# Optimization experiments

Measured on AMD Instinct MI355X. Metric: run time of the kernel, lower is better.

## Reference

```python
import jax, jax.numpy as jnp
import numpy as np

H = 64  # hidden_size
IN = 1  # input_size
OUT = 32  # fc output


def _lstm_layer(x, Wih, Whh, bih, bhh):
    """x: (B,T,D_in). Returns (outputs (B,T,H), final h (B,H)). PyTorch gate order i,f,g,o."""
    B = x.shape[0]
    b = bih + bhh  # (4H,)
    # precompute input contributions for all timesteps: (T,B,4H)
    xW = jnp.einsum('btd,gd->tbg', x, Wih) + b

    def step(carry, xw_t):
        h, c = carry
        gates = xw_t + h @ Whh.T  # (B,4H)
        i, f, g, o = jnp.split(gates, 4, axis=-1)
        i = jax.nn.sigmoid(i)
        f = jax.nn.sigmoid(f)
        g = jnp.tanh(g)
        o = jax.nn.sigmoid(o)
        c = f * c + i * g
        h = o * jnp.tanh(c)
        return (h, c), h

    h0 = jnp.zeros((B, H), dtype=x.dtype)
    c0 = jnp.zeros((B, H), dtype=x.dtype)
    (h_T, _), hs = jax.lax.scan(step, (h0, c0), xW)
    return jnp.swapaxes(hs, 0, 1), h_T


def setup_inputs() -> dict:
    key = jax.random.key(0)
    ks = jax.random.split(key, 11)
    s_ih0 = 1.0 / np.sqrt(H)
    inp = {
        'x': jax.random.normal(ks[0], (2048, 512, IN), dtype=jnp.float32),
        # layer 0: input_size -> H
        'Wih0': jax.random.uniform(ks[1], (4 * H, IN), minval=-s_ih0, maxval=s_ih0),
        'Whh0': jax.random.uniform(ks[2], (4 * H, H), minval=-s_ih0, maxval=s_ih0),
        'bih0': jax.random.uniform(ks[3], (4 * H,), minval=-s_ih0, maxval=s_ih0),
        'bhh0': jax.random.uniform(ks[4], (4 * H,), minval=-s_ih0, maxval=s_ih0),
        # layer 1: H -> H
        'Wih1': jax.random.uniform(ks[5], (4 * H, H), minval=-s_ih0, maxval=s_ih0),
        'Whh1': jax.random.uniform(ks[6], (4 * H, H), minval=-s_ih0, maxval=s_ih0),
        'bih1': jax.random.uniform(ks[7], (4 * H,), minval=-s_ih0, maxval=s_ih0),
        'bhh1': jax.random.uniform(ks[8], (4 * H,), minval=-s_ih0, maxval=s_ih0),
        # fc: H -> 32
        'fcW': jax.random.uniform(ks[9], (OUT, H), minval=-s_ih0, maxval=s_ih0),
        'fcb': jax.random.uniform(ks[10], (OUT,), minval=-s_ih0, maxval=s_ih0),
    }
    return inp


def reference(x, Wih0, Whh0, bih0, bhh0, Wih1, Whh1, bih1, bhh1, fcW, fcb):
    h1_seq, _ = _lstm_layer(x, Wih0, Whh0, bih0, bhh0)
    _, h_last = _lstm_layer(h1_seq, Wih1, Whh1, bih1, bhh1)  # hidden[-1]
    features = jax.nn.relu(h_last @ fcW.T + fcb)  # (B, 32)
    return features
```

## Files before the change

kernel.cpp:

```cpp
#include <hip/hip_runtime.h>
#include <hip/hip_bf16.h>


#define HID 64
#define TSTEPS 512
#define MB 8
#define RS 80

typedef _Float16 f16x8 __attribute__((ext_vector_type(8)));
typedef float f32x4 __attribute__((ext_vector_type(4)));

#define KSIG (-1.44269504089f)
#define KTANH (2.88539008178f)

__device__ __forceinline__ float sig1(float p) {
    return __builtin_amdgcn_rcpf(1.f + __builtin_amdgcn_exp2f(p));
}
__device__ __forceinline__ float th1(float p) {
    return 1.f - 2.f * __builtin_amdgcn_rcpf(1.f + __builtin_amdgcn_exp2f(p));
}

__global__ __launch_bounds__(512, 1) void lstm_feat_kernel(
    const float* __restrict__ x,
    const float* __restrict__ Wih0, const float* __restrict__ Whh0,
    const float* __restrict__ bih0, const float* __restrict__ bhh0,
    const float* __restrict__ Wih1, const float* __restrict__ Whh1,
    const float* __restrict__ bih1, const float* __restrict__ bhh1,
    const float* __restrict__ fcW, const float* __restrict__ fcb,
    float* __restrict__ out)
{
    __shared__ float x_lds[(MB / 2) * TSTEPS * 2];
    __shared__ __align__(16) _Float16 h0_lds[4][MB * RS];
    __shared__ __align__(16) _Float16 h1_lds[2][MB * RS];
    __shared__ float h1f32[MB * HID];
    __shared__ float fcw_lds[HID * 32];
    __shared__ float fcb_lds[32];

    const int tid  = threadIdx.x;
    const int wave = tid >> 6;
    const int lane = tid & 63;
    const int nq   = lane & 15;
    const int quad = lane >> 4;
    const int bbase = blockIdx.x * MB;
    const bool isL1 = (wave >= 4);
    const int ug = wave & 3;
    const int u  = ug * 16 + nq;

    for (int i = tid; i < TSTEPS * MB; i += 512) {
        int r = i >> 9, t = i & (TSTEPS - 1);
        x_lds[(r >> 1) * (TSTEPS * 2) + t * 2 + (r & 1)] = x[(bbase + r) * TSTEPS + t];
    }
    for (int i = tid; i < 32 * HID; i += 512) {
        int o = i >> 6, kk = i & 63;
        fcw_lds[kk * 32 + o] = fcW[i];
    }
    if (tid < 32) fcb_lds[tid] = fcb[tid];
    for (int i = tid; i < 4 * MB * RS; i += 512) ((_Float16*)h0_lds)[i] = (_Float16)0.f;
    for (int i = tid; i < 2 * MB * RS; i += 512) ((_Float16*)h1_lds)[i] = (_Float16)0.f;

    f16x8 wA[4][2], wB[4][2];
    f32x4 cbias[4];
    float bsc[4], wx0s[4];
    {
        const float* Wa = isL1 ? Wih1 : Whh0;
        const float* Wb = isL1 ? Whh1 : Whh0;
        const float* bi = isL1 ? bih1 : bih0;
        const float* bh = isL1 ? bhh1 : bhh0;
        #pragma unroll
        for (int g = 0; g < 4; ++g) {
            const float sc = (g == 2) ? KTANH : KSIG;
            const int n = g * 64 + u;
            const float bs = (bi[n] + bh[n]) * sc;
            bsc[g] = bs;
            cbias[g] = (f32x4){bs, bs, bs, bs};
            wx0s[g] = Wih0[n] * sc;
            #pragma unroll
            for (int ks = 0; ks < 2; ++ks) {
                const int k0 = quad * 8 + ks * 32;
                f16x8 a, b;
                #pragma unroll
                for (int j = 0; j < 8; ++j) {
                    a[j] = (_Float16)(Wa[n * HID + k0 + j] * sc);
                    b[j] = (_Float16)(Wb[n * HID + k0 + j] * sc);
                }
                wA[g][ks] = a; wB[g][ks] = b;
            }
        }
    }

    const int arow = (nq >> 1) * RS + quad * 8;
    const int b0r  = (quad * 2) * RS;
    const int hbase = quad * 2;
    float c0 = 0.f, c1 = 0.f;
    f32x4 accA[4] = { {0,0,0,0},{0,0,0,0},{0,0,0,0},{0,0,0,0} };

    __syncthreads();

#define CELL(AC, DST) do {                                                        \
    float i0 = sig1(AC[0][0]), i1 = sig1(AC[0][2]);                               \
    float f0 = sig1(AC[1][0]), f1 = sig1(AC[1][2]);                               \
    float g0 = th1(AC[2][0]),  g1 = th1(AC[2][2]);                                \
    float o0 = sig1(AC[3][0]), o1 = sig1(AC[3][2]);                               \
    c0 = f0 * c0 + i0 * g0;  c1 = f1 * c1 + i1 * g1;                              \
    float t0 = th1(c0 * KTANH), t1 = th1(c1 * KTANH);                             \
    (DST)[b0r + u]      = (_Float16)(o0 * t0);                                    \
    (DST)[b0r + RS + u] = (_Float16)(o1 * t1);                                    \
} while (0)

#define L0_STEP(P, Q, XA, XB) do {                                                \
    f16x8 a0 = *(const f16x8*)&h0_lds[P][arow];                                   \
    f16x8 a1 = *(const f16x8*)&h0_lds[P][arow + 32];                              \
    f32x4 ac[4];                                                                  \
    __builtin_amdgcn_s_setprio(1);                                                \
    _Pragma("unroll")                                                             \
    for (int g = 0; g < 4; ++g) {                                                 \
        f32x4 Cg;                                                                 \
        Cg[0] = fmaf((XA), wx0s[g], bsc[g]); Cg[1] = bsc[g];                      \
        Cg[2] = fmaf((XB), wx0s[g], bsc[g]); Cg[3] = bsc[g];                      \
        ac[g] = __builtin_amdgcn_mfma_f32_16x16x32_f16(a0, wA[g][0], Cg, 0, 0, 0);\
    }                                                                             \
    _Pragma("unroll")                                                             \
    for (int g = 0; g < 4; ++g)                                                   \
        ac[g] = __builtin_amdgcn_mfma_f32_16x16x32_f16(a1, wA[g][1], ac[g], 0, 0, 0); \
    __builtin_amdgcn_s_setprio(0);                                                \
    CELL(ac, h0_lds[Q]);                                                          \
} while (0)

#define L1_STEP(RB, WRB, PF) do {                                                 \
    f16x8 b0v = *(const f16x8*)&h1_lds[RB][arow];                                 \
    f16x8 b1v = *(const f16x8*)&h1_lds[RB][arow + 32];                            \
    f16x8 p0 = *(const f16x8*)&h0_lds[PF][arow];                                  \
    f16x8 p1 = *(const f16x8*)&h0_lds[PF][arow + 32];                             \
    f32x4 ac[4];                                                                  \
    __builtin_amdgcn_s_setprio(1);                                                \
    _Pragma("unroll")                                                             \
    for (int g = 0; g < 4; ++g)                                                   \
        ac[g] = __builtin_amdgcn_mfma_f32_16x16x32_f16(b0v, wB[g][0], accA[g], 0, 0, 0); \
    _Pragma("unroll")                                                             \
    for (int g = 0; g < 4; ++g)                                                   \
        ac[g] = __builtin_amdgcn_mfma_f32_16x16x32_f16(b1v, wB[g][1], ac[g], 0, 0, 0);   \
    __builtin_amdgcn_s_setprio(0);                                                \
    _Pragma("unroll")                                                             \
    for (int g = 0; g < 4; ++g)                                                   \
        accA[g] = __builtin_amdgcn_mfma_f32_16x16x32_f16(p0, wA[g][0], cbias[g], 0, 0, 0); \
    _Pragma("unroll")                                                             \
    for (int g = 0; g < 4; ++g)                                                   \
        accA[g] = __builtin_amdgcn_mfma_f32_16x16x32_f16(p1, wA[g][1], accA[g], 0, 0, 0);  \
    CELL(ac, h1_lds[WRB]);                                                        \
} while (0)

#define L1_PF(PF) do {                                                            \
    f16x8 p0 = *(const f16x8*)&h0_lds[PF][arow];                                  \
    f16x8 p1 = *(const f16x8*)&h0_lds[PF][arow + 32];                             \
    _Pragma("unroll")                                                             \
    for (int g = 0; g < 4; ++g)                                                   \
        accA[g] = __builtin_amdgcn_mfma_f32_16x16x32_f16(p0, wA[g][0], cbias[g], 0, 0, 0); \
    _Pragma("unroll")                                                             \
    for (int g = 0; g < 4; ++g)                                                   \
        accA[g] = __builtin_amdgcn_mfma_f32_16x16x32_f16(p1, wA[g][1], accA[g], 0, 0, 0);  \
} while (0)

    const int xoff = quad * (TSTEPS * 2);

    {
        const f32x4 xv0 = *(const f32x4*)&x_lds[xoff + 0];
        const f32x4 xv1 = *(const f32x4*)&x_lds[xoff + 4];
        if (!isL1) L0_STEP(0, 1, xv0[0], xv0[1]); else L1_PF(0);
        __syncthreads();
        if (!isL1) L0_STEP(1, 2, xv0[2], xv0[3]); else L1_PF(1);
        __syncthreads();
        if (!isL1) L0_STEP(2, 3, xv1[0], xv1[1]); else L1_STEP(0, 1, 2);
        __syncthreads();
        if (!isL1) L0_STEP(3, 0, xv1[2], xv1[3]); else L1_STEP(1, 0, 3);
        __syncthreads();
    }

    for (int k = 4; k < TSTEPS; k += 4) {
        const f32x4 xv0 = *(const f32x4*)&x_lds[xoff + k * 2];
        const f32x4 xv1 = *(const f32x4*)&x_lds[xoff + k * 2 + 4];
        if (!isL1) L0_STEP(0, 1, xv0[0], xv0[1]); else L1_STEP(0, 1, 0);
        __syncthreads();
        if (!isL1) L0_STEP(1, 2, xv0[2], xv0[3]); else L1_STEP(1, 0, 1);
        __syncthreads();
        if (!isL1) L0_STEP(2, 3, xv1[0], xv1[1]); else L1_STEP(0, 1, 2);
        __syncthreads();
        if (!isL1) L0_STEP(3, 0, xv1[2], xv1[3]); else L1_STEP(1, 0, 3);
        __syncthreads();
    }

    if (isL1) {
        f16x8 b0v = *(const f16x8*)&h1_lds[0][arow];
        f16x8 b1v = *(const f16x8*)&h1_lds[0][arow + 32];
        f32x4 ac[4];
        #pragma unroll
        for (int g = 0; g < 4; ++g)
            ac[g] = __builtin_amdgcn_mfma_f32_16x16x32_f16(b0v, wB[g][0], accA[g], 0, 0, 0);
        #pragma unroll
        for (int g = 0; g < 4; ++g)
            ac[g] = __builtin_amdgcn_mfma_f32_16x16x32_f16(b1v, wB[g][1], ac[g], 0, 0, 0);
        CELL(ac, h1_lds[1]);
    }
    __syncthreads();

    if (isL1) {
        f16x8 p0  = *(const f16x8*)&h0_lds[0][arow];
        f16x8 p1  = *(const f16x8*)&h0_lds[0][arow + 32];
        f16x8 b0v = *(const f16x8*)&h1_lds[1][arow];
        f16x8 b1v = *(const f16x8*)&h1_lds[1][arow + 32];
        f32x4 ac[4];
        #pragma unroll
        for (int g = 0; g < 4; ++g)
            ac[g] = __builtin_amdgcn_mfma_f32_16x16x32_f16(p0, wA[g][0], cbias[g], 0, 0, 0);
        #pragma unroll
        for (int g = 0; g < 4; ++g)
            ac[g] = __builtin_amdgcn_mfma_f32_16x16x32_f16(p1, wA[g][1], ac[g], 0, 0, 0);
        #pragma unroll
        for (int g = 0; g < 4; ++g)
            ac[g] = __builtin_amdgcn_mfma_f32_16x16x32_f16(b0v, wB[g][0], ac[g], 0, 0, 0);
        #pragma unroll
        for (int g = 0; g < 4; ++g)
            ac[g] = __builtin_amdgcn_mfma_f32_16x16x32_f16(b1v, wB[g][1], ac[g], 0, 0, 0);
        float i0 = sig1(ac[0][0]), i1 = sig1(ac[0][2]);
        float f0 = sig1(ac[1][0]), f1 = sig1(ac[1][2]);
        float g0 = th1(ac[2][0]),  g1 = th1(ac[2][2]);
        float o0 = sig1(ac[3][0]), o1 = sig1(ac[3][2]);
        c0 = f0 * c0 + i0 * g0;  c1 = f1 * c1 + i1 * g1;
        h1f32[hbase * HID + u]       = o0 * th1(c0 * KTANH);
        h1f32[(hbase + 1) * HID + u] = o1 * th1(c1 * KTANH);
    }
    __syncthreads();

    if (tid < MB * 32) {
        const int o  = tid & 31;
        const int rr = tid >> 5;
        float acc = fcb_lds[o];
        #pragma unroll 8
        for (int kk = 0; kk < HID; ++kk)
            acc += h1f32[rr * HID + kk] * fcw_lds[kk * 32 + o];
        out[(bbase + rr) * 32 + o] = fmaxf(acc, 0.f);
    }
}

extern "C" void kernel_launch(void* const* d_in, const int* in_sizes, int n_in,
                              void* d_out, int out_size, void* d_ws, size_t ws_size,
                              hipStream_t stream) {
    const float* x    = (const float*)d_in[0];
    const float* Wih0 = (const float*)d_in[1];
    const float* Whh0 = (const float*)d_in[2];
    const float* bih0 = (const float*)d_in[3];
    const float* bhh0 = (const float*)d_in[4];
    const float* Wih1 = (const float*)d_in[5];
    const float* Whh1 = (const float*)d_in[6];
    const float* bih1 = (const float*)d_in[7];
    const float* bhh1 = (const float*)d_in[8];
    const float* fcW  = (const float*)d_in[9];
    const float* fcb  = (const float*)d_in[10];
    float* out = (float*)d_out;

    lstm_feat_kernel<<<2048 / MB, 512, 0, stream>>>(
        x, Wih0, Whh0, bih0, bhh0, Wih1, Whh1, bih1, bhh1, fcW, fcb, out);
}
```

Baseline: 312.7 us.

## Halve batch rows per block to double grid and allow multiple blocks per CU

Reduces the batch tile from 8 to 4 sequences per block, so each MFMA row group is replicated across 4 A-rows and each lane handles one cell instead of two. This doubles the grid size (512 blocks), and launch_bounds is raised to 4 blocks per SM, so more independent recurrences can overlap on each CU and hide the serial latency of the time loop. The cost is more redundant MFMA work per useful row, since the 16-row tiles now carry only 4 distinct sequences, and possible register pressure under the tighter occupancy bound.

```diff
diff --git a/kernel.cpp b/kernel.cpp
--- a/kernel.cpp
+++ b/kernel.cpp
@@ -4,7 +4,7 @@
 
 #define HID 64
 #define TSTEPS 512
-#define MB 8
+#define MB 4
 #define RS 80
 
 typedef _Float16 f16x8 __attribute__((ext_vector_type(8)));
@@ -20,7 +20,7 @@
     return 1.f - 2.f * __builtin_amdgcn_rcpf(1.f + __builtin_amdgcn_exp2f(p));
 }
 
-__global__ __launch_bounds__(512, 1) void lstm_feat_kernel(
+__global__ __launch_bounds__(512, 4) void lstm_feat_kernel(
     const float* __restrict__ x,
     const float* __restrict__ Wih0, const float* __restrict__ Whh0,
     const float* __restrict__ bih0, const float* __restrict__ bhh0,
@@ -29,7 +29,7 @@
     const float* __restrict__ fcW, const float* __restrict__ fcb,
     float* __restrict__ out)
 {
-    __shared__ float x_lds[(MB / 2) * TSTEPS * 2];
+    __shared__ __align__(16) float x_lds[MB * TSTEPS];
     __shared__ __align__(16) _Float16 h0_lds[4][MB * RS];
     __shared__ __align__(16) _Float16 h1_lds[2][MB * RS];
     __shared__ float h1f32[MB * HID];
@@ -46,9 +46,9 @@
     const int ug = wave & 3;
     const int u  = ug * 16 + nq;
 
-    for (int i = tid; i < TSTEPS * MB; i += 512) {
+    for (int i = tid; i < MB * TSTEPS; i += 512) {
         int r = i >> 9, t = i & (TSTEPS - 1);
-        x_lds[(r >> 1) * (TSTEPS * 2) + t * 2 + (r & 1)] = x[(bbase + r) * TSTEPS + t];
+        x_lds[r * TSTEPS + t] = x[(bbase + r) * TSTEPS + t];
     }
     for (int i = tid; i < 32 * HID; i += 512) {
         int o = i >> 6, kk = i & 63;
@@ -88,42 +88,37 @@
         }
     }
 
-    const int arow = (nq >> 1) * RS + quad * 8;
-    const int b0r  = (quad * 2) * RS;
-    const int hbase = quad * 2;
-    float c0 = 0.f, c1 = 0.f;
+    const int arow = (nq >> 2) * RS + quad * 8;
+    float c0 = 0.f;
     f32x4 accA[4] = { {0,0,0,0},{0,0,0,0},{0,0,0,0},{0,0,0,0} };
 
     __syncthreads();
 
-#define CELL(AC, DST) do {                                                        \
-    float i0 = sig1(AC[0][0]), i1 = sig1(AC[0][2]);                               \
-    float f0 = sig1(AC[1][0]), f1 = sig1(AC[1][2]);                               \
-    float g0 = th1(AC[2][0]),  g1 = th1(AC[2][2]);                                \
-    float o0 = sig1(AC[3][0]), o1 = sig1(AC[3][2]);                               \
-    c0 = f0 * c0 + i0 * g0;  c1 = f1 * c1 + i1 * g1;                              \
-    float t0 = th1(c0 * KTANH), t1 = th1(c1 * KTANH);                             \
-    (DST)[b0r + u]      = (_Float16)(o0 * t0);                                    \
-    (DST)[b0r + RS + u] = (_Float16)(o1 * t1);                                    \
-} while (0)
-
-#define L0_STEP(P, Q, XA, XB) do {                                                \
+#define CELL1(AC, DST) do {                                                       \
+    float iv = sig1(AC[0][0]);                                                    \
+    float fv = sig1(AC[1][0]);                                                    \
+    float gv = th1(AC[2][0]);                                                     \
+    float ov = sig1(AC[3][0]);                                                    \
+    c0 = fv * c0 + iv * gv;                                                       \
+    (DST)[quad * RS + u] = (_Float16)(ov * th1(c0 * KTANH));                      \
+} while (0)
+
+#define L0_STEP(P, Q, XS) do {                                                    \
     f16x8 a0 = *(const f16x8*)&h0_lds[P][arow];                                   \
     f16x8 a1 = *(const f16x8*)&h0_lds[P][arow + 32];                              \
     f32x4 ac[4];                                                                  \
     __builtin_amdgcn_s_setprio(1);                                                \
     _Pragma("unroll")                                                             \
     for (int g = 0; g < 4; ++g) {                                                 \
-        f32x4 Cg;                                                                 \
-        Cg[0] = fmaf((XA), wx0s[g], bsc[g]); Cg[1] = bsc[g];                      \
-        Cg[2] = fmaf((XB), wx0s[g], bsc[g]); Cg[3] = bsc[g];                      \
+        const float cv = fmaf((XS), wx0s[g], bsc[g]);                             \
+        f32x4 Cg = {cv, cv, cv, cv};                                              \
         ac[g] = __builtin_amdgcn_mfma_f32_16x16x32_f16(a0, wA[g][0], Cg, 0, 0, 0);\
     }                                                                             \
     _Pragma("unroll")                                                             \
     for (int g = 0; g < 4; ++g)                                                   \
         ac[g] = __builtin_amdgcn_mfma_f32_16x16x32_f16(a1, wA[g][1], ac[g], 0, 0, 0); \
     __builtin_amdgcn_s_setprio(0);                                                \
-    CELL(ac, h0_lds[Q]);                                                          \
+    CELL1(ac, h0_lds[Q]);                                                         \
 } while (0)
 
 #define L1_STEP(RB, WRB, PF) do {                                                 \
@@ -146,7 +141,7 @@
     _Pragma("unroll")                                                             \
     for (int g = 0; g < 4; ++g)                                                   \
         accA[g] = __builtin_amdgcn_mfma_f32_16x16x32_f16(p1, wA[g][1], accA[g], 0, 0, 0);  \
-    CELL(ac, h1_lds[WRB]);                                                        \
+    CELL1(ac, h1_lds[WRB]);                                                       \
 } while (0)
 
 #define L1_PF(PF) do {                                                            \
@@ -160,31 +155,29 @@
         accA[g] = __builtin_amdgcn_mfma_f32_16x16x32_f16(p1, wA[g][1], accA[g], 0, 0, 0);  \
 } while (0)
 
-    const int xoff = quad * (TSTEPS * 2);
+    const int xoff = quad * TSTEPS;
 
     {
-        const f32x4 xv0 = *(const f32x4*)&x_lds[xoff + 0];
-        const f32x4 xv1 = *(const f32x4*)&x_lds[xoff + 4];
-        if (!isL1) L0_STEP(0, 1, xv0[0], xv0[1]); else L1_PF(0);
-        __syncthreads();
-        if (!isL1) L0_STEP(1, 2, xv0[2], xv0[3]); else L1_PF(1);
-        __syncthreads();
-        if (!isL1) L0_STEP(2, 3, xv1[0], xv1[1]); else L1_STEP(0, 1, 2);
-        __syncthreads();
-        if (!isL1) L0_STEP(3, 0, xv1[2], xv1[3]); else L1_STEP(1, 0, 3);
+        const f32x4 xv = *(const f32x4*)&x_lds[xoff];
+        if (!isL1) L0_STEP(0, 1, xv[0]); else L1_PF(0);
+        __syncthreads();
+        if (!isL1) L0_STEP(1, 2, xv[1]); else L1_PF(1);
+        __syncthreads();
+        if (!isL1) L0_STEP(2, 3, xv[2]); else L1_STEP(0, 1, 2);
+        __syncthreads();
+        if (!isL1) L0_STEP(3, 0, xv[3]); else L1_STEP(1, 0, 3);
         __syncthreads();
     }
 
     for (int k = 4; k < TSTEPS; k += 4) {
-        const f32x4 xv0 = *(const f32x4*)&x_lds[xoff + k * 2];
-        const f32x4 xv1 = *(const f32x4*)&x_lds[xoff + k * 2 + 4];
-        if (!isL1) L0_STEP(0, 1, xv0[0], xv0[1]); else L1_STEP(0, 1, 0);
-        __syncthreads();
-        if (!isL1) L0_STEP(1, 2, xv0[2], xv0[3]); else L1_STEP(1, 0, 1);
-        __syncthreads();
-        if (!isL1) L0_STEP(2, 3, xv1[0], xv1[1]); else L1_STEP(0, 1, 2);
-        __syncthreads();
-        if (!isL1) L0_STEP(3, 0, xv1[2], xv1[3]); else L1_STEP(1, 0, 3);
+        const f32x4 xv = *(const f32x4*)&x_lds[xoff + k];
+        if (!isL1) L0_STEP(0, 1, xv[0]); else L1_STEP(0, 1, 0);
+        __syncthreads();
+        if (!isL1) L0_STEP(1, 2, xv[1]); else L1_STEP(1, 0, 1);
+        __syncthreads();
+        if (!isL1) L0_STEP(2, 3, xv[2]); else L1_STEP(0, 1, 2);
+        __syncthreads();
+        if (!isL1) L0_STEP(3, 0, xv[3]); else L1_STEP(1, 0, 3);
         __syncthreads();
     }
 
@@ -198,7 +191,7 @@
         #pragma unroll
         for (int g = 0; g < 4; ++g)
             ac[g] = __builtin_amdgcn_mfma_f32_16x16x32_f16(b1v, wB[g][1], ac[g], 0, 0, 0);
-        CELL(ac, h1_lds[1]);
+        CELL1(ac, h1_lds[1]);
     }
     __syncthreads();
 
@@ -220,13 +213,12 @@
         #pragma unroll
         for (int g = 0; g < 4; ++g)
             ac[g] = __builtin_amdgcn_mfma_f32_16x16x32_f16(b1v, wB[g][1], ac[g], 0, 0, 0);
-        float i0 = sig1(ac[0][0]), i1 = sig1(ac[0][2]);
-        float f0 = sig1(ac[1][0]), f1 = sig1(ac[1][2]);
-        float g0 = th1(ac[2][0]),  g1 = th1(ac[2][2]);
-        float o0 = sig1(ac[3][0]), o1 = sig1(ac[3][2]);
-        c0 = f0 * c0 + i0 * g0;  c1 = f1 * c1 + i1 * g1;
-        h1f32[hbase * HID + u]       = o0 * th1(c0 * KTANH);
-        h1f32[(hbase + 1) * HID + u] = o1 * th1(c1 * KTANH);
+        float iv = sig1(ac[0][0]);
+        float fv = sig1(ac[1][0]);
+        float gv = th1(ac[2][0]);
+        float ov = sig1(ac[3][0]);
+        c0 = fv * c0 + iv * gv;
+        h1f32[quad * HID + u] = ov * th1(c0 * KTANH);
     }
     __syncthreads();
 
```

Result: slower. 509.5 us (+62.9%).

## Split LSTM steps into MFMA and cell phases interleaved across layers

Applied to the files above, without the earlier changes.

Each timestep is split into two half-phases separated by barriers. Layer-0 waves run MFMA while layer-1 waves run gate nonlinearities, and the reverse in the next half-phase, so the matrix and transcendental units are meant to overlap across wave groups. Layer 1 now computes both its input and recurrent products in one phase instead of prefetching the input product a step ahead. This doubles the number of block-wide barriers per timestep, which adds synchronisation overhead in exchange for the overlap.

```diff
diff --git a/kernel.cpp b/kernel.cpp
--- a/kernel.cpp
+++ b/kernel.cpp
@@ -19,6 +19,8 @@
 __device__ __forceinline__ float th1(float p) {
     return 1.f - 2.f * __builtin_amdgcn_rcpf(1.f + __builtin_amdgcn_exp2f(p));
 }
+
+#define MFMA16(A, B, C) __builtin_amdgcn_mfma_f32_16x16x32_f16((A), (B), (C), 0, 0, 0)
 
 __global__ __launch_bounds__(512, 1) void lstm_feat_kernel(
     const float* __restrict__ x,
@@ -29,7 +31,7 @@
     const float* __restrict__ fcW, const float* __restrict__ fcb,
     float* __restrict__ out)
 {
-    __shared__ float x_lds[(MB / 2) * TSTEPS * 2];
+    __shared__ __align__(16) float x_lds[(MB / 2) * TSTEPS * 2];
     __shared__ __align__(16) _Float16 h0_lds[4][MB * RS];
     __shared__ __align__(16) _Float16 h1_lds[2][MB * RS];
     __shared__ float h1f32[MB * HID];
@@ -60,10 +62,9 @@
 
     f16x8 wA[4][2], wB[4][2];
     f32x4 cbias[4];
-    float bsc[4], wx0s[4];
+    float wx0s[4];
     {
         const float* Wa = isL1 ? Wih1 : Whh0;
-        const float* Wb = isL1 ? Whh1 : Whh0;
         const float* bi = isL1 ? bih1 : bih0;
         const float* bh = isL1 ? bhh1 : bhh0;
         #pragma unroll
@@ -71,19 +72,32 @@
             const float sc = (g == 2) ? KTANH : KSIG;
             const int n = g * 64 + u;
             const float bs = (bi[n] + bh[n]) * sc;
-            bsc[g] = bs;
             cbias[g] = (f32x4){bs, bs, bs, bs};
             wx0s[g] = Wih0[n] * sc;
             #pragma unroll
             for (int ks = 0; ks < 2; ++ks) {
                 const int k0 = quad * 8 + ks * 32;
-                f16x8 a, b;
+                f16x8 a;
                 #pragma unroll
-                for (int j = 0; j < 8; ++j) {
+                for (int j = 0; j < 8; ++j)
                     a[j] = (_Float16)(Wa[n * HID + k0 + j] * sc);
-                    b[j] = (_Float16)(Wb[n * HID + k0 + j] * sc);
+                wA[g][ks] = a;
+            }
+        }
+        if (isL1) {
+            #pragma unroll
+            for (int g = 0; g < 4; ++g) {
+                const float sc = (g == 2) ? KTANH : KSIG;
+                const int n = g * 64 + u;
+                #pragma unroll
+                for (int ks = 0; ks < 2; ++ks) {
+                    const int k0 = quad * 8 + ks * 32;
+                    f16x8 b;
+                    #pragma unroll
+                    for (int j = 0; j < 8; ++j)
+                        b[j] = (_Float16)(Whh1[n * HID + k0 + j] * sc);
+                    wB[g][ks] = b;
                 }
-                wA[g][ks] = a; wB[g][ks] = b;
             }
         }
     }
@@ -92,72 +106,65 @@
     const int b0r  = (quad * 2) * RS;
     const int hbase = quad * 2;
     float c0 = 0.f, c1 = 0.f;
-    f32x4 accA[4] = { {0,0,0,0},{0,0,0,0},{0,0,0,0},{0,0,0,0} };
-
-    __syncthreads();
-
-#define CELL(AC, DST) do {                                                        \
-    float i0 = sig1(AC[0][0]), i1 = sig1(AC[0][2]);                               \
-    float f0 = sig1(AC[1][0]), f1 = sig1(AC[1][2]);                               \
-    float g0 = th1(AC[2][0]),  g1 = th1(AC[2][2]);                                \
-    float o0 = sig1(AC[3][0]), o1 = sig1(AC[3][2]);                               \
-    c0 = f0 * c0 + i0 * g0;  c1 = f1 * c1 + i1 * g1;                              \
-    float t0 = th1(c0 * KTANH), t1 = th1(c1 * KTANH);                             \
-    (DST)[b0r + u]      = (_Float16)(o0 * t0);                                    \
-    (DST)[b0r + RS + u] = (_Float16)(o1 * t1);                                    \
-} while (0)
-
-#define L0_STEP(P, Q, XA, XB) do {                                                \
-    f16x8 a0 = *(const f16x8*)&h0_lds[P][arow];                                   \
-    f16x8 a1 = *(const f16x8*)&h0_lds[P][arow + 32];                              \
-    f32x4 ac[4];                                                                  \
+    f32x4 l0ac[4], l1ac[4];
+
+    __syncthreads();
+
+#define L0A(S) do {                                                               \
+    f16x8 a0 = *(const f16x8*)&h0_lds[S][arow];                                   \
+    f16x8 a1 = *(const f16x8*)&h0_lds[S][arow + 32];                              \
     __builtin_amdgcn_s_setprio(1);                                                \
     _Pragma("unroll")                                                             \
-    for (int g = 0; g < 4; ++g) {                                                 \
-        f32x4 Cg;                                                                 \
-        Cg[0] = fmaf((XA), wx0s[g], bsc[g]); Cg[1] = bsc[g];                      \
-        Cg[2] = fmaf((XB), wx0s[g], bsc[g]); Cg[3] = bsc[g];                      \
-        ac[g] = __builtin_amdgcn_mfma_f32_16x16x32_f16(a0, wA[g][0], Cg, 0, 0, 0);\
-    }                                                                             \
-    _Pragma("unroll")                                                             \
-    for (int g = 0; g < 4; ++g)                                                   \
-        ac[g] = __builtin_amdgcn_mfma_f32_16x16x32_f16(a1, wA[g][1], ac[g], 0, 0, 0); \
+    for (int g = 0; g < 4; ++g) l0ac[g] = MFMA16(a0, wA[g][0], cbias[g]);         \
+    _Pragma("unroll")                                                             \
+    for (int g = 0; g < 4; ++g) l0ac[g] = MFMA16(a1, wA[g][1], l0ac[g]);          \
     __builtin_amdgcn_s_setprio(0);                                                \
-    CELL(ac, h0_lds[Q]);                                                          \
-} while (0)
-
-#define L1_STEP(RB, WRB, PF) do {                                                 \
-    f16x8 b0v = *(const f16x8*)&h1_lds[RB][arow];                                 \
-    f16x8 b1v = *(const f16x8*)&h1_lds[RB][arow + 32];                            \
-    f16x8 p0 = *(const f16x8*)&h0_lds[PF][arow];                                  \
-    f16x8 p1 = *(const f16x8*)&h0_lds[PF][arow + 32];                             \
-    f32x4 ac[4];                                                                  \
+} while (0)
+
+#define L0B(Q, XA, XB) do {                                                       \
+    float pi0 = fmaf((XA), wx0s[0], l0ac[0][0]), pi1 = fmaf((XB), wx0s[0], l0ac[0][2]); \
+    float pf0 = fmaf((XA), wx0s[1], l0ac[1][0]), pf1 = fmaf((XB), wx0s[1], l0ac[1][2]); \
+    float pg0 = fmaf((XA), wx0s[2], l0ac[2][0]), pg1 = fmaf((XB), wx0s[2], l0ac[2][2]); \
+    float po0 = fmaf((XA), wx0s[3], l0ac[3][0]), po1 = fmaf((XB), wx0s[3], l0ac[3][2]); \
+    float iv0 = sig1(pi0), iv1 = sig1(pi1), fv0 = sig1(pf0), fv1 = sig1(pf1);     \
+    float gv0 = th1(pg0),  gv1 = th1(pg1),  ov0 = sig1(po0), ov1 = sig1(po1);     \
+    c0 = fmaf(fv0, c0, iv0 * gv0);  c1 = fmaf(fv1, c1, iv1 * gv1);                \
+    h0_lds[Q][b0r + u]      = (_Float16)(ov0 * th1(c0 * KTANH));                  \
+    h0_lds[Q][b0r + RS + u] = (_Float16)(ov1 * th1(c1 * KTANH));                  \
+} while (0)
+
+#define L1A(H1S) do {                                                             \
+    float iv0 = sig1(l1ac[0][0]), iv1 = sig1(l1ac[0][2]);                         \
+    float fv0 = sig1(l1ac[1][0]), fv1 = sig1(l1ac[1][2]);                         \
+    float gv0 = th1(l1ac[2][0]),  gv1 = th1(l1ac[2][2]);                          \
+    float ov0 = sig1(l1ac[3][0]), ov1 = sig1(l1ac[3][2]);                         \
+    c0 = fmaf(fv0, c0, iv0 * gv0);  c1 = fmaf(fv1, c1, iv1 * gv1);                \
+    h1_lds[H1S][b0r + u]      = (_Float16)(ov0 * th1(c0 * KTANH));                \
+    h1_lds[H1S][b0r + RS + u] = (_Float16)(ov1 * th1(c1 * KTANH));                \
+} while (0)
+
+#define L1B(SH0, H1S) do {                                                        \
+    f16x8 a00 = *(const f16x8*)&h0_lds[SH0][arow];                                \
+    f16x8 a01 = *(const f16x8*)&h0_lds[SH0][arow + 32];                           \
+    f16x8 a10 = *(const f16x8*)&h1_lds[H1S][arow];                                \
+    f16x8 a11 = *(const f16x8*)&h1_lds[H1S][arow + 32];                           \
     __builtin_amdgcn_s_setprio(1);                                                \
     _Pragma("unroll")                                                             \
-    for (int g = 0; g < 4; ++g)                                                   \
-        ac[g] = __builtin_amdgcn_mfma_f32_16x16x32_f16(b0v, wB[g][0], accA[g], 0, 0, 0); \
-    _Pragma("unroll")                                                             \
-    for (int g = 0; g < 4; ++g)                                                   \
-        ac[g] = __builtin_amdgcn_mfma_f32_16x16x32_f16(b1v, wB[g][1], ac[g], 0, 0, 0);   \
+    for (int g = 0; g < 4; ++g) l1ac[g] = MFMA16(a00, wA[g][0], cbias[g]);        \
+    _Pragma("unroll")                                                             \
+    for (int g = 0; g < 4; ++g) l1ac[g] = MFMA16(a01, wA[g][1], l1ac[g]);         \
+    _Pragma("unroll")                                                             \
+    for (int g = 0; g < 4; ++g) l1ac[g] = MFMA16(a10, wB[g][0], l1ac[g]);         \
+    _Pragma("unroll")                                                             \
+    for (int g = 0; g < 4; ++g) l1ac[g] = MFMA16(a11, wB[g][1], l1ac[g]);         \
     __builtin_amdgcn_s_setprio(0);                                                \
-    _Pragma("unroll")                                                             \
-    for (int g = 0; g < 4; ++g)                                                   \
-        accA[g] = __builtin_amdgcn_mfma_f32_16x16x32_f16(p0, wA[g][0], cbias[g], 0, 0, 0); \
-    _Pragma("unroll")                                                             \
-    for (int g = 0; g < 4; ++g)                                                   \
-        accA[g] = __builtin_amdgcn_mfma_f32_16x16x32_f16(p1, wA[g][1], accA[g], 0, 0, 0);  \
-    CELL(ac, h1_lds[WRB]);                                                        \
-} while (0)
-
-#define L1_PF(PF) do {                                                            \
-    f16x8 p0 = *(const f16x8*)&h0_lds[PF][arow];                                  \
-    f16x8 p1 = *(const f16x8*)&h0_lds[PF][arow + 32];                             \
-    _Pragma("unroll")                                                             \
-    for (int g = 0; g < 4; ++g)                                                   \
-        accA[g] = __builtin_amdgcn_mfma_f32_16x16x32_f16(p0, wA[g][0], cbias[g], 0, 0, 0); \
-    _Pragma("unroll")                                                             \
-    for (int g = 0; g < 4; ++g)                                                   \
-        accA[g] = __builtin_amdgcn_mfma_f32_16x16x32_f16(p1, wA[g][1], accA[g], 0, 0, 0);  \
+} while (0)
+
+#define IV(S, H1S, XA, XB, DOA, DOB) do {                                         \
+    if (!isL1) { L0A(S); } else if (DOA) { L1A(H1S); }                            \
+    __syncthreads();                                                              \
+    if (!isL1) { L0B((S + 1) & 3, XA, XB); } else if (DOB) { L1B((S + 3) & 3, H1S); } \
+    __syncthreads();                                                              \
 } while (0)
 
     const int xoff = quad * (TSTEPS * 2);
@@ -165,68 +172,38 @@
     {
         const f32x4 xv0 = *(const f32x4*)&x_lds[xoff + 0];
         const f32x4 xv1 = *(const f32x4*)&x_lds[xoff + 4];
-        if (!isL1) L0_STEP(0, 1, xv0[0], xv0[1]); else L1_PF(0);
-        __syncthreads();
-        if (!isL1) L0_STEP(1, 2, xv0[2], xv0[3]); else L1_PF(1);
-        __syncthreads();
-        if (!isL1) L0_STEP(2, 3, xv1[0], xv1[1]); else L1_STEP(0, 1, 2);
-        __syncthreads();
-        if (!isL1) L0_STEP(3, 0, xv1[2], xv1[3]); else L1_STEP(1, 0, 3);
-        __syncthreads();
-    }
-
-    for (int k = 4; k < TSTEPS; k += 4) {
-        const f32x4 xv0 = *(const f32x4*)&x_lds[xoff + k * 2];
-        const f32x4 xv1 = *(const f32x4*)&x_lds[xoff + k * 2 + 4];
-        if (!isL1) L0_STEP(0, 1, xv0[0], xv0[1]); else L1_STEP(0, 1, 0);
-        __syncthreads();
-        if (!isL1) L0_STEP(1, 2, xv0[2], xv0[3]); else L1_STEP(1, 0, 1);
-        __syncthreads();
-        if (!isL1) L0_STEP(2, 3, xv1[0], xv1[1]); else L1_STEP(0, 1, 2);
-        __syncthreads();
-        if (!isL1) L0_STEP(3, 0, xv1[2], xv1[3]); else L1_STEP(1, 0, 3);
-        __syncthreads();
-    }
+        IV(0, 0, xv0[0], xv0[1], false, false);
+        IV(1, 1, xv0[2], xv0[3], false, false);
+        IV(2, 0, xv1[0], xv1[1], false, true);
+        IV(3, 1, xv1[2], xv1[3], true,  true);
+    }
+
+    for (int n = 4; n < TSTEPS; n += 4) {
+        const f32x4 xv0 = *(const f32x4*)&x_lds[xoff + n * 2];
+        const f32x4 xv1 = *(const f32x4*)&x_lds[xoff + n * 2 + 4];
+        IV(0, 0, xv0[0], xv0[1], true, true);
+        IV(1, 1, xv0[2], xv0[3], true, true);
+        IV(2, 0, xv1[0], xv1[1], true, true);
+        IV(3, 1, xv1[2], xv1[3], true, true);
+    }
+
+    if (isL1) L1A(0);
+    __syncthreads();
+    if (isL1) L1B(3, 0);
+    __syncthreads();
+    if (isL1) L1A(1);
+    __syncthreads();
+    if (isL1) L1B(0, 1);
+    __syncthreads();
 
     if (isL1) {
-        f16x8 b0v = *(const f16x8*)&h1_lds[0][arow];
-        f16x8 b1v = *(const f16x8*)&h1_lds[0][arow + 32];
-        f32x4 ac[4];
-        #pragma unroll
-        for (int g = 0; g < 4; ++g)
-            ac[g] = __builtin_amdgcn_mfma_f32_16x16x32_f16(b0v, wB[g][0], accA[g], 0, 0, 0);
-        #pragma unroll
-        for (int g = 0; g < 4; ++g)
-            ac[g] = __builtin_amdgcn_mfma_f32_16x16x32_f16(b1v, wB[g][1], ac[g], 0, 0, 0);
-        CELL(ac, h1_lds[1]);
-    }
-    __syncthreads();
-
-    if (isL1) {
-        f16x8 p0  = *(const f16x8*)&h0_lds[0][arow];
-        f16x8 p1  = *(const f16x8*)&h0_lds[0][arow + 32];
-        f16x8 b0v = *(const f16x8*)&h1_lds[1][arow];
-        f16x8 b1v = *(const f16x8*)&h1_lds[1][arow + 32];
-        f32x4 ac[4];
-        #pragma unroll
-        for (int g = 0; g < 4; ++g)
-            ac[g] = __builtin_amdgcn_mfma_f32_16x16x32_f16(p0, wA[g][0], cbias[g], 0, 0, 0);
-        #pragma unroll
-        for (int g = 0; g < 4; ++g)
-            ac[g] = __builtin_amdgcn_mfma_f32_16x16x32_f16(p1, wA[g][1], ac[g], 0, 0, 0);
-        #pragma unroll
-        for (int g = 0; g < 4; ++g)
-            ac[g] = __builtin_amdgcn_mfma_f32_16x16x32_f16(b0v, wB[g][0], ac[g], 0, 0, 0);
-        #pragma unroll
-        for (int g = 0; g < 4; ++g)
-            ac[g] = __builtin_amdgcn_mfma_f32_16x16x32_f16(b1v, wB[g][1], ac[g], 0, 0, 0);
-        float i0 = sig1(ac[0][0]), i1 = sig1(ac[0][2]);
-        float f0 = sig1(ac[1][0]), f1 = sig1(ac[1][2]);
-        float g0 = th1(ac[2][0]),  g1 = th1(ac[2][2]);
-        float o0 = sig1(ac[3][0]), o1 = sig1(ac[3][2]);
-        c0 = f0 * c0 + i0 * g0;  c1 = f1 * c1 + i1 * g1;
-        h1f32[hbase * HID + u]       = o0 * th1(c0 * KTANH);
-        h1f32[(hbase + 1) * HID + u] = o1 * th1(c1 * KTANH);
+        float iv0 = sig1(l1ac[0][0]), iv1 = sig1(l1ac[0][2]);
+        float fv0 = sig1(l1ac[1][0]), fv1 = sig1(l1ac[1][2]);
+        float gv0 = th1(l1ac[2][0]),  gv1 = th1(l1ac[2][2]);
+        float ov0 = sig1(l1ac[3][0]), ov1 = sig1(l1ac[3][2]);
+        c0 = fmaf(fv0, c0, iv0 * gv0);  c1 = fmaf(fv1, c1, iv1 * gv1);
+        h1f32[hbase * HID + u]       = ov0 * th1(c0 * KTANH);
+        h1f32[(hbase + 1) * HID + u] = ov1 * th1(c1 * KTANH);
     }
     __syncthreads();
 
```

Result: slower. 337.8 us (+8.0%).
